# Kernel tuning notes

Measured on AMD Instinct MI355X. Metric: run time of the kernel, lower is better.

## Reference

```python
import jax, jax.numpy as jnp
import numpy as np

B, L, D = 2, 2048, 2560
H, KV, HD = 8, 4, 256
FF = 10240
WINDOW = 1024
ROPE_BASE = 10000.0
EPS = 1e-6


def rmsnorm(x, scale=None):
    x32 = x.astype(jnp.float32)
    var = jnp.mean(jnp.square(x32), axis=-1, keepdims=True)
    xn = x32 * jax.lax.rsqrt(var + EPS)
    return xn if scale is None else xn * scale.astype(jnp.float32)


def apply_rope(x, positions, base):
    # full RoPE (rope_fraction=1.0): rotate pairs (i, i+head_dim//2)
    hd = x.shape[-1]
    half = hd // 2
    timescale = base ** (2.0 * jnp.arange(half, dtype=jnp.float32) / hd)
    ang = positions[:, :, None].astype(jnp.float32) / timescale  # [B,L,half]
    sin = jnp.sin(ang)[:, :, None, :]  # [B,L,1,half]
    cos = jnp.cos(ang)[:, :, None, :]
    x1, x2 = x[..., :half], x[..., half:]
    return jnp.concatenate([x1 * cos - x2 * sin, x2 * cos + x1 * sin], axis=-1)


def setup_inputs() -> dict:
    key = jax.random.key(0)
    ks = jax.random.split(key, 16)
    s = lambda fan_in: 1.0 / np.sqrt(fan_in)
    return {
        "x": jax.random.normal(ks[0], (B, L, D), jnp.float32),
        "positions": jnp.broadcast_to(jnp.arange(L, dtype=jnp.int32), (B, L)),
        "wq": jax.random.normal(ks[1], (D, H * HD), jnp.float32) * s(D),
        "wk": jax.random.normal(ks[2], (D, KV * HD), jnp.float32) * s(D),
        "wv": jax.random.normal(ks[3], (D, KV * HD), jnp.float32) * s(D),
        "wo": jax.random.normal(ks[4], (H * HD, D), jnp.float32) * s(H * HD),
        "q_scale": jnp.ones((HD,), jnp.float32),
        "k_scale": jnp.ones((HD,), jnp.float32),
        "pre_attn_scale": jnp.ones((D,), jnp.float32),
        "post_attn_scale": jnp.ones((D,), jnp.float32),
        "pre_ffw_scale": jnp.ones((D,), jnp.float32),
        "post_ffw_scale": jnp.ones((D,), jnp.float32),
        "w_gate": jax.random.normal(ks[5], (D, FF), jnp.float32) * s(D),
        "w_up": jax.random.normal(ks[6], (D, FF), jnp.float32) * s(D),
        "w_down": jax.random.normal(ks[7], (FF, D), jnp.float32) * s(FF),
    }


def reference(x, positions, wq, wk, wv, wo, q_scale, k_scale,
              pre_attn_scale, post_attn_scale, pre_ffw_scale, post_ffw_scale,
              w_gate, w_up, w_down):
    # --- attention sub-block ---
    h = rmsnorm(x, pre_attn_scale)
    q = (h @ wq).reshape(B, L, H, HD)
    k = (h @ wk).reshape(B, L, KV, HD)
    v = (h @ wv).reshape(B, L, KV, HD)
    q = apply_rope(rmsnorm(q, q_scale), positions, ROPE_BASE)
    k = apply_rope(rmsnorm(k, k_scale), positions, ROPE_BASE)
    v = rmsnorm(v)  # RMSNormNoScale on V
    rep = H // KV
    k = jnp.repeat(k, rep, axis=2)  # [B,L,H,HD]
    v = jnp.repeat(v, rep, axis=2)
    scores = jnp.einsum("bqhd,bkhd->bhqk", q, k)  # NOTE: no 1/sqrt(d) scaling, faithful to source
    i = jnp.arange(L)[:, None]
    j = jnp.arange(L)[None, :]
    mask = (j <= i) & (j > i - WINDOW)  # causal & sliding window
    scores = jnp.where(mask[None, None, :, :], scores, -10000.0)
    probs = jax.nn.softmax(scores.astype(jnp.float32), axis=-1)
    attn = jnp.einsum("bhqk,bkhd->bqhd", probs, v).reshape(B, L, H * HD)
    attn = attn @ wo
    x = x + rmsnorm(attn, post_attn_scale)
    # --- feedforward sub-block (GeGLU) ---
    h = rmsnorm(x, pre_ffw_scale)
    hidden = jax.nn.gelu(h @ w_gate, approximate=False) * (h @ w_up)
    ffw = hidden @ w_down
    x = x + rmsnorm(ffw, post_ffw_scale)
    return x
```

## Files before the change

kernel.cpp:

```cpp
#include <hip/hip_runtime.h>
#include <math.h>

#define DEV __device__ __forceinline__

typedef _Float16 f16;
typedef _Float16 f16x8 __attribute__((ext_vector_type(8)));
typedef _Float16 f16x4 __attribute__((ext_vector_type(4)));
typedef float f32x4 __attribute__((ext_vector_type(4)));

DEV void gload_lds16(const void* g, void* l) {
  __builtin_amdgcn_global_load_lds(
      (const __attribute__((address_space(1))) void*)g,
      (__attribute__((address_space(3))) void*)l, 16, 0, 0);
}

__global__ void transpose_w(const float* __restrict__ src, f16* __restrict__ dst,
                            int R, int C) {
  __shared__ float tile[32][33];
  int c0 = blockIdx.x * 32, r0 = blockIdx.y * 32;
  int tx = threadIdx.x, ty = threadIdx.y;
#pragma unroll
  for (int j = 0; j < 32; j += 8)
    tile[ty + j][tx] = src[(size_t)(r0 + ty + j) * C + c0 + tx];
  __syncthreads();
#pragma unroll
  for (int j = 0; j < 32; j += 8)
    dst[(size_t)(c0 + ty + j) * R + r0 + tx] = (f16)tile[tx][ty + j];
}

__global__ void rope_table_k(float* __restrict__ tab) {
  int idx = blockIdx.x * 256 + threadIdx.x;
  int pos = idx >> 7, j = idx & 127;
  float ts = powf(10000.0f, (float)j * (1.0f / 128.0f));
  float ang = (float)pos / ts;
  tab[pos * 256 + j] = sinf(ang);
  tab[pos * 256 + 128 + j] = cosf(ang);
}

__global__ __launch_bounds__(256) void rmsnorm_f32_f16(
    const float* __restrict__ in, const float* __restrict__ scale,
    f16* __restrict__ out) {
  constexpr int D = 2560, N4 = D / 4;
  const int m = blockIdx.x, tid = threadIdx.x;
  const float* row = in + (size_t)m * D;
  float vals[12];
  float ss = 0.f;
#pragma unroll
  for (int it = 0; it < 3; ++it) {
    int c4 = tid + it * 256;
    if (c4 < N4) {
      float4 v = *(const float4*)(row + c4 * 4);
      vals[it * 4 + 0] = v.x; vals[it * 4 + 1] = v.y;
      vals[it * 4 + 2] = v.z; vals[it * 4 + 3] = v.w;
      ss += v.x * v.x + v.y * v.y + v.z * v.z + v.w * v.w;
    }
  }
#pragma unroll
  for (int off = 32; off; off >>= 1) ss += __shfl_xor(ss, off, 64);
  __shared__ float red[4];
  if ((tid & 63) == 0) red[tid >> 6] = ss;
  __syncthreads();
  float rs = rsqrtf((red[0] + red[1] + red[2] + red[3]) * (1.0f / D) + 1e-6f);
#pragma unroll
  for (int it = 0; it < 3; ++it) {
    int c4 = tid + it * 256;
    if (c4 < N4) {
      float4 sc = *(const float4*)(scale + c4 * 4);
      f16x4 o;
      o[0] = (f16)(vals[it * 4 + 0] * rs * sc.x);
      o[1] = (f16)(vals[it * 4 + 1] * rs * sc.y);
      o[2] = (f16)(vals[it * 4 + 2] * rs * sc.z);
      o[3] = (f16)(vals[it * 4 + 3] * rs * sc.w);
      *(f16x4*)(out + (size_t)m * D + c4 * 4) = o;
    }
  }
}

__global__ __launch_bounds__(256) void residual_rmsnorm(
    const float* x, const f16* __restrict__ y,
    const float* __restrict__ scale, float* out) {
  constexpr int D = 2560, N4 = D / 4;
  const int m = blockIdx.x, tid = threadIdx.x;
  const f16* yr = y + (size_t)m * D;
  float yv[12];
  float ss = 0.f;
#pragma unroll
  for (int it = 0; it < 3; ++it) {
    int c4 = tid + it * 256;
    if (c4 < N4) {
      f16x4 u = *(const f16x4*)(yr + c4 * 4);
      float a = (float)u[0], b = (float)u[1], c = (float)u[2], d = (float)u[3];
      yv[it * 4 + 0] = a; yv[it * 4 + 1] = b; yv[it * 4 + 2] = c; yv[it * 4 + 3] = d;
      ss += a * a + b * b + c * c + d * d;
    }
  }
#pragma unroll
  for (int off = 32; off; off >>= 1) ss += __shfl_xor(ss, off, 64);
  __shared__ float red[4];
  if ((tid & 63) == 0) red[tid >> 6] = ss;
  __syncthreads();
  float rs = rsqrtf((red[0] + red[1] + red[2] + red[3]) * (1.0f / D) + 1e-6f);
#pragma unroll
  for (int it = 0; it < 3; ++it) {
    int c4 = tid + it * 256;
    if (c4 < N4) {
      float4 xv = *(const float4*)(x + (size_t)m * D + c4 * 4);
      float4 sc = *(const float4*)(scale + c4 * 4);
      float4 o;
      o.x = xv.x + yv[it * 4 + 0] * rs * sc.x;
      o.y = xv.y + yv[it * 4 + 1] * rs * sc.y;
      o.z = xv.z + yv[it * 4 + 2] * rs * sc.z;
      o.w = xv.w + yv[it * 4 + 3] * rs * sc.w;
      *(float4*)(out + (size_t)m * D + c4 * 4) = o;
    }
  }
}

__global__ __launch_bounds__(256) void norm_rope_k(
    const f16* __restrict__ qkv, const int* __restrict__ positions,
    const float* __restrict__ q_scale, const float* __restrict__ k_scale,
    const float* __restrict__ tab,
    f16* __restrict__ q_g, f16* __restrict__ k_g, f16* __restrict__ v_n) {
  const int m = blockIdx.x;
  const int tid = threadIdx.x, w = tid >> 6, l = tid & 63;
  const int pos = positions[m];
  const float* srow = tab + (size_t)pos * 256;
  const int c0 = l * 4;
  for (int vi = w; vi < 16; vi += 4) {
    f16x4 u = *(const f16x4*)(qkv + (size_t)m * 4096 + vi * 256 + c0);
    float x0 = (float)u[0], x1 = (float)u[1], x2 = (float)u[2], x3 = (float)u[3];
    float ss = x0 * x0 + x1 * x1 + x2 * x2 + x3 * x3;
#pragma unroll
    for (int off = 32; off; off >>= 1) ss += __shfl_xor(ss, off, 64);
    float rs = rsqrtf(ss * (1.0f / 256.0f) + 1e-6f);
    if (vi < 12) {
      const float* sc = (vi < 8) ? q_scale : k_scale;
      float4 s4 = *(const float4*)(sc + c0);
      float n0 = x0 * rs * s4.x, n1 = x1 * rs * s4.y;
      float n2 = x2 * rs * s4.z, n3 = x3 * rs * s4.w;
      float p0 = __shfl_xor(n0, 32, 64), p1 = __shfl_xor(n1, 32, 64);
      float p2 = __shfl_xor(n2, 32, 64), p3 = __shfl_xor(n3, 32, 64);
      int j0 = c0 & 127;
      float4 sn = *(const float4*)(srow + j0);
      float4 cs = *(const float4*)(srow + 128 + j0);
      float sgn = (l < 32) ? -1.0f : 1.0f;
      f16x4 o;
      o[0] = (f16)(n0 * cs.x + sgn * p0 * sn.x);
      o[1] = (f16)(n1 * cs.y + sgn * p1 * sn.y);
      o[2] = (f16)(n2 * cs.z + sgn * p2 * sn.z);
      o[3] = (f16)(n3 * cs.w + sgn * p3 * sn.w);
      if (vi < 8) *(f16x4*)(q_g + (size_t)m * 2048 + vi * 256 + c0) = o;
      else        *(f16x4*)(k_g + (size_t)m * 1024 + (vi - 8) * 256 + c0) = o;
    } else {
      f16x4 o;
      o[0] = (f16)(x0 * rs); o[1] = (f16)(x1 * rs);
      o[2] = (f16)(x2 * rs); o[3] = (f16)(x3 * rs);
      *(f16x4*)(v_n + (size_t)m * 1024 + (vi - 12) * 256 + c0) = o;
    }
  }
}

__global__ void transpose_v_k(const f16* __restrict__ v_n, f16* __restrict__ vt) {
  __shared__ f16 tile[32][33];
  int bkv = blockIdx.z;
  int b = bkv >> 2, kv = bkv & 3;
  int t0 = blockIdx.x * 32, d0 = blockIdx.y * 32;
  int tx = threadIdx.x, ty = threadIdx.y;
#pragma unroll
  for (int j = 0; j < 32; j += 8)
    tile[ty + j][tx] =
        v_n[(size_t)(b * 2048 + t0 + ty + j) * 1024 + kv * 256 + d0 + tx];
  __syncthreads();
#pragma unroll
  for (int j = 0; j < 32; j += 8)
    vt[((size_t)bkv * 256 + d0 + ty + j) * 2048 + t0 + tx] = tile[tx][ty + j];
}

template <int EPI>
__global__ void gemm_bt(const f16* __restrict__ A, const f16* __restrict__ BT,
                        f16* C, const f16* aux, int M, int N, int K) {
  constexpr int BM = 128, BN = 128, BK = 64;
  __shared__ f16 As[BM * BK];
  __shared__ f16 Bs[BN * BK];
  const int tid = threadIdx.x;
  const int w = tid >> 6, l = tid & 63;
  const int l15 = l & 15, lk = l >> 4;
  const int bn = blockIdx.x, bm = blockIdx.y;
  const int wm = (w >> 1) * 64, wn = (w & 1) * 64;

  f32x4 acc[4][4] = {};

  const size_t abase = (size_t)(bm * BM) * K;
  const size_t bbase = (size_t)(bn * BN) * K;
  const int r = tid >> 3, cc = (tid & 7) * 8;

  for (int kt = 0; kt < K; kt += BK) {
#pragma unroll
    for (int it = 0; it < 4; ++it) {
      int rr = r + it * 32;
      gload_lds16(A + abase + (size_t)rr * K + kt + cc, &As[rr * BK + cc]);
      gload_lds16(BT + bbase + (size_t)rr * K + kt + cc, &Bs[rr * BK + cc]);
    }
    __syncthreads();
#pragma unroll
    for (int ks = 0; ks < 2; ++ks) {
      f16x8 af[4], bfr[4];
#pragma unroll
      for (int mi = 0; mi < 4; ++mi)
        af[mi] = *(const f16x8*)&As[(wm + mi * 16 + l15) * BK + ks * 32 + lk * 8];
#pragma unroll
      for (int ni = 0; ni < 4; ++ni)
        bfr[ni] = *(const f16x8*)&Bs[(wn + ni * 16 + l15) * BK + ks * 32 + lk * 8];
#pragma unroll
      for (int mi = 0; mi < 4; ++mi)
#pragma unroll
        for (int ni = 0; ni < 4; ++ni)
          acc[mi][ni] = __builtin_amdgcn_mfma_f32_16x16x32_f16(
              af[mi], bfr[ni], acc[mi][ni], 0, 0, 0);
    }
    __syncthreads();
  }
#pragma unroll
  for (int mi = 0; mi < 4; ++mi) {
#pragma unroll
    for (int ni = 0; ni < 4; ++ni) {
#pragma unroll
      for (int i = 0; i < 4; ++i) {
        int row = bm * BM + wm + mi * 16 + lk * 4 + i;
        int col = bn * BN + wn + ni * 16 + l15;
        size_t idx = (size_t)row * N + col;
        float v = acc[mi][ni][i];
        if constexpr (EPI == 1) {
          v = 0.5f * v * (1.0f + erff(v * 0.70710678118654752f));
        } else if constexpr (EPI == 2) {
          v *= (float)aux[idx];
        }
        C[idx] = (f16)v;
      }
    }
  }
}

__global__ __launch_bounds__(256) void flash_attn_k(
    const f16* __restrict__ q_g, const f16* __restrict__ k_g,
    const f16* __restrict__ vt, f16* __restrict__ ctx) {
  constexpr int KP = 264, VP = 40, PP = 40;
  __shared__ f16 Ks[32 * KP];
  __shared__ f16 Vs[256 * VP];
  __shared__ f16 Ps[4][16 * PP];
  const int qt = blockIdx.x, h = blockIdx.y, b = blockIdx.z;
  const int tid = threadIdx.x, w = tid >> 6, l = tid & 63;
  const int l15 = l & 15, lk = l >> 4;
  const int kv = h >> 1;

  f16x8 aq[8];
  const int qrow = qt * 64 + w * 16 + l15;
  const f16* qp = q_g + (size_t)(b * 2048 + qrow) * 2048 + h * 256 + lk * 8;
#pragma unroll
  for (int kc = 0; kc < 8; ++kc) aq[kc] = *(const f16x8*)(qp + kc * 32);

  f32x4 o[16] = {};
  float mrow[4] = {-1e30f, -1e30f, -1e30f, -1e30f};
  float lrow[4] = {0.f, 0.f, 0.f, 0.f};

  int kt_lo = 2 * qt - 32; if (kt_lo < 0) kt_lo = 0;
  const int kt_hi = 2 * qt + 1;
  const int iqb = qt * 64 + w * 16 + lk * 4;

  for (int kt = kt_lo; kt <= kt_hi; ++kt) {
    __syncthreads();
#pragma unroll
    for (int it = 0; it < 4; ++it) {
      int ch = tid + it * 256;
      int jl = ch >> 5, kcc = (ch & 31) * 8;
      *(f16x8*)&Ks[jl * KP + kcc] = *(const f16x8*)(
          k_g + (size_t)(b * 2048 + kt * 32 + jl) * 1024 + kv * 256 + kcc);
      int d = ch >> 2, tc = (ch & 3) * 8;
      *(f16x8*)&Vs[d * VP + tc] = *(const f16x8*)(
          vt + ((size_t)(b * 4 + kv) * 256 + d) * 2048 + kt * 32 + tc);
    }
    __syncthreads();
    f32x4 s[2] = {};
#pragma unroll
    for (int ct = 0; ct < 2; ++ct)
#pragma unroll
      for (int kc = 0; kc < 8; ++kc) {
        f16x8 bk = *(const f16x8*)&Ks[(ct * 16 + l15) * KP + kc * 32 + lk * 8];
        s[ct] = __builtin_amdgcn_mfma_f32_16x16x32_f16(aq[kc], bk, s[ct], 0, 0, 0);
      }
    float pm[4] = {-1e30f, -1e30f, -1e30f, -1e30f};
#pragma unroll
    for (int ct = 0; ct < 2; ++ct)
#pragma unroll
      for (int i = 0; i < 4; ++i) {
        int iq = iqb + i;
        int j = kt * 32 + ct * 16 + l15;
        bool valid = (j <= iq) && (j > iq - 1024);
        float sv = valid ? s[ct][i] : -1e30f;
        s[ct][i] = sv;
        pm[i] = fmaxf(pm[i], sv);
      }
#pragma unroll
    for (int i = 0; i < 4; ++i)
#pragma unroll
      for (int off = 1; off < 16; off <<= 1)
        pm[i] = fmaxf(pm[i], __shfl_xor(pm[i], off, 64));
    float corr[4], rsum[4];
#pragma unroll
    for (int i = 0; i < 4; ++i) {
      float mn = fmaxf(mrow[i], pm[i]);
      corr[i] = __expf(mrow[i] - mn);
      mrow[i] = mn;
      rsum[i] = 0.f;
    }
#pragma unroll
    for (int ct = 0; ct < 2; ++ct)
#pragma unroll
      for (int i = 0; i < 4; ++i) {
        float p = (s[ct][i] > -1e29f) ? __expf(s[ct][i] - mrow[i]) : 0.f;
        s[ct][i] = p;
        rsum[i] += p;
      }
#pragma unroll
    for (int i = 0; i < 4; ++i) {
#pragma unroll
      for (int off = 1; off < 16; off <<= 1) rsum[i] += __shfl_xor(rsum[i], off, 64);
      lrow[i] = lrow[i] * corr[i] + rsum[i];
    }
#pragma unroll
    for (int dt = 0; dt < 16; ++dt)
#pragma unroll
      for (int i = 0; i < 4; ++i) o[dt][i] *= corr[i];
#pragma unroll
    for (int ct = 0; ct < 2; ++ct)
#pragma unroll
      for (int i = 0; i < 4; ++i)
        Ps[w][(lk * 4 + i) * PP + ct * 16 + l15] = (f16)s[ct][i];
    __syncthreads();
    f16x8 pa = *(const f16x8*)&Ps[w][l15 * PP + lk * 8];
#pragma unroll
    for (int dt = 0; dt < 16; ++dt) {
      f16x8 bv = *(const f16x8*)&Vs[(dt * 16 + l15) * VP + lk * 8];
      o[dt] = __builtin_amdgcn_mfma_f32_16x16x32_f16(pa, bv, o[dt], 0, 0, 0);
    }
  }
  float inv[4];
#pragma unroll
  for (int i = 0; i < 4; ++i) inv[i] = 1.0f / lrow[i];
  f16* op = ctx + (size_t)(b * 2048 + qt * 64 + w * 16 + lk * 4) * 2048 + h * 256 + l15;
#pragma unroll
  for (int dt = 0; dt < 16; ++dt)
#pragma unroll
    for (int i = 0; i < 4; ++i)
      op[(size_t)i * 2048 + dt * 16] = (f16)(o[dt][i] * inv[i]);
}

extern "C" void kernel_launch(void* const* d_in, const int* in_sizes, int n_in,
                              void* d_out, int out_size, void* d_ws, size_t ws_size,
                              hipStream_t stream) {
  const float* x = (const float*)d_in[0];
  const int* positions = (const int*)d_in[1];
  const float* wq = (const float*)d_in[2];
  const float* wk = (const float*)d_in[3];
  const float* wv = (const float*)d_in[4];
  const float* wo = (const float*)d_in[5];
  const float* q_scale = (const float*)d_in[6];
  const float* k_scale = (const float*)d_in[7];
  const float* pre_attn = (const float*)d_in[8];
  const float* post_attn = (const float*)d_in[9];
  const float* pre_ffw = (const float*)d_in[10];
  const float* post_ffw = (const float*)d_in[11];
  const float* w_gate = (const float*)d_in[12];
  const float* w_up = (const float*)d_in[13];
  const float* w_down = (const float*)d_in[14];
  float* out = (float*)d_out;

  char* ws = (char*)d_ws;
  size_t off = 0;
  auto alloc = [&](size_t bytes) {
    char* p = ws + off;
    off += (bytes + 255) & ~(size_t)255;
    return p;
  };
  f16* wbuf = (f16*)alloc((size_t)10240 * 2560 * 2);
  float* tab = (float*)alloc((size_t)2048 * 256 * 4);
  f16* h     = (f16*)alloc((size_t)4096 * 2560 * 2);
  char* act  = alloc((size_t)92280832);
  f16* qkv    = (f16*)(act);
  f16* q_g    = (f16*)(act + (size_t)33554432);
  f16* k_g    = (f16*)(act + (size_t)33554432 + 16777216);
  f16* v_n    = (f16*)(act + (size_t)33554432 + 16777216 + 8388608);
  f16* vtb    = (f16*)(act + (size_t)33554432 + 16777216 + 2 * 8388608);
  f16* ctx    = (f16*)(act + (size_t)33554432 + 16777216 + 3 * 8388608);
  f16* attn_o = (f16*)(act);
  f16* gbuf = (f16*)(act);
  f16* ffw  = h;
  (void)in_sizes; (void)n_in; (void)out_size; (void)ws_size;

  dim3 tb(32, 8);
  rope_table_k<<<1024, 256, 0, stream>>>(tab);

  rmsnorm_f32_f16<<<4096, 256, 0, stream>>>(x, pre_attn, h);
  transpose_w<<<dim3(2048 / 32, 2560 / 32), tb, 0, stream>>>(wq, wbuf, 2560, 2048);
  transpose_w<<<dim3(1024 / 32, 2560 / 32), tb, 0, stream>>>(wk, wbuf + (size_t)2048 * 2560, 2560, 1024);
  transpose_w<<<dim3(1024 / 32, 2560 / 32), tb, 0, stream>>>(wv, wbuf + (size_t)3072 * 2560, 2560, 1024);
  gemm_bt<0><<<dim3(4096 / 128, 4096 / 128), 256, 0, stream>>>(h, wbuf, qkv, nullptr, 4096, 4096, 2560);
  norm_rope_k<<<4096, 256, 0, stream>>>(qkv, positions, q_scale, k_scale, tab, q_g, k_g, v_n);
  transpose_v_k<<<dim3(2048 / 32, 256 / 32, 8), tb, 0, stream>>>(v_n, vtb);
  flash_attn_k<<<dim3(32, 8, 2), 256, 0, stream>>>(q_g, k_g, vtb, ctx);
  transpose_w<<<dim3(2560 / 32, 2048 / 32), tb, 0, stream>>>(wo, wbuf, 2048, 2560);
  gemm_bt<0><<<dim3(2560 / 128, 4096 / 128), 256, 0, stream>>>(ctx, wbuf, attn_o, nullptr, 4096, 2560, 2048);
  residual_rmsnorm<<<4096, 256, 0, stream>>>(x, attn_o, post_attn, out);

  rmsnorm_f32_f16<<<4096, 256, 0, stream>>>(out, pre_ffw, h);
  transpose_w<<<dim3(10240 / 32, 2560 / 32), tb, 0, stream>>>(w_gate, wbuf, 2560, 10240);
  gemm_bt<1><<<dim3(10240 / 128, 4096 / 128), 256, 0, stream>>>(h, wbuf, gbuf, nullptr, 4096, 10240, 2560);
  transpose_w<<<dim3(10240 / 32, 2560 / 32), tb, 0, stream>>>(w_up, wbuf, 2560, 10240);
  gemm_bt<2><<<dim3(10240 / 128, 4096 / 128), 256, 0, stream>>>(h, wbuf, gbuf, gbuf, 4096, 10240, 2560);
  transpose_w<<<dim3(2560 / 32, 10240 / 32), tb, 0, stream>>>(w_down, wbuf, 10240, 2560);
  gemm_bt<0><<<dim3(2560 / 128, 4096 / 128), 256, 0, stream>>>(gbuf, wbuf, ffw, nullptr, 4096, 2560, 10240);
  residual_rmsnorm<<<4096, 256, 0, stream>>>(out, ffw, post_ffw, out);
}
```

Baseline: 1.291 ms.

## Replace 128x128 GEMM with pipelined 256x256 tile kernel using swizzled LDS

Replaces the simple 128x128 single-buffered GEMM with a 256x256-tile, 512-thread kernel. It uses 128KB of double-buffered dynamic LDS, an XOR-swizzled LDS layout, and staged async global-to-LDS loads interleaved with MFMA phases. It also adds a workgroup index swizzle for L2 locality and setprio around MFMA blocks. The goal is to hide global load latency, cut LDS bank conflicts and raise MFMA utilization across all projection and FFN GEMMs. The trade-off is fewer, larger workgroups (e.g. 160 blocks for N=2560) and heavy register and LDS pressure.

Measured after the change: 1.239 ms. -4.0%, faster.

```diff
diff --git a/kernel.cpp b/kernel.cpp
--- a/kernel.cpp
+++ b/kernel.cpp
@@ -177,57 +177,126 @@
 }
 
 template <int EPI>
-__global__ void gemm_bt(const f16* __restrict__ A, const f16* __restrict__ BT,
-                        f16* C, const f16* aux, int M, int N, int K) {
-  constexpr int BM = 128, BN = 128, BK = 64;
-  __shared__ f16 As[BM * BK];
-  __shared__ f16 Bs[BN * BK];
+__global__ __launch_bounds__(512, 2) void gemm256(
+    const f16* __restrict__ A, const f16* __restrict__ BT,
+    f16* __restrict__ C, const f16* __restrict__ aux, int M, int N, int K) {
+  extern __shared__ __align__(16) f16 lds[];
   const int tid = threadIdx.x;
   const int w = tid >> 6, l = tid & 63;
   const int l15 = l & 15, lk = l >> 4;
-  const int bn = blockIdx.x, bm = blockIdx.y;
-  const int wm = (w >> 1) * 64, wn = (w & 1) * 64;
-
-  f32x4 acc[4][4] = {};
-
-  const size_t abase = (size_t)(bm * BM) * K;
-  const size_t bbase = (size_t)(bn * BN) * K;
-  const int r = tid >> 3, cc = (tid & 7) * 8;
-
-  for (int kt = 0; kt < K; kt += BK) {
-#pragma unroll
-    for (int it = 0; it < 4; ++it) {
-      int rr = r + it * 32;
-      gload_lds16(A + abase + (size_t)rr * K + kt + cc, &As[rr * BK + cc]);
-      gload_lds16(BT + bbase + (size_t)rr * K + kt + cc, &Bs[rr * BK + cc]);
-    }
-    __syncthreads();
-#pragma unroll
-    for (int ks = 0; ks < 2; ++ks) {
-      f16x8 af[4], bfr[4];
-#pragma unroll
-      for (int mi = 0; mi < 4; ++mi)
-        af[mi] = *(const f16x8*)&As[(wm + mi * 16 + l15) * BK + ks * 32 + lk * 8];
+  const int wm = w >> 2, wn = w & 3;
+
+  const int gx = gridDim.x;
+  const int nwg = gx * gridDim.y;
+  const int orig = blockIdx.y * gx + blockIdx.x;
+  const int swz = (orig & 7) * (nwg >> 3) + (orig >> 3);
+  const int bn = swz % gx, bm = swz / gx;
+
+  const f16* Ab = A + (size_t)bm * 256 * K;
+  const f16* Bb = BT + (size_t)bn * 256 * K;
+  const int NT = K >> 6;
+
+  const int srow = tid >> 2;
+  const int sg = (tid & 3) ^ ((srow >> 1) & 3);
+
+  auto stage = [&](int op, int kh, int buf, int kt) {
+    const f16* src = (op ? Bb : Ab) + (size_t)srow * K + kt * 64 + kh * 32 + sg * 8;
+    f16* dst = lds + ((buf << 2) + (kh << 1) + op) * 8192 + tid * 8;
+    gload_lds16(src, dst);
+    gload_lds16(src + (size_t)128 * K, dst + 4096);
+  };
+
+  const int fcol = (lk ^ ((l15 >> 1) & 3)) << 3;
+  const int aoff = (wm * 128 + l15) * 32 + fcol;
+  const int boff = 8192 + (wn * 64 + l15) * 32 + fcol;
+
+  f32x4 acc[8][4] = {};
+
+  stage(0, 0, 0, 0);
+  stage(1, 0, 0, 0);
+  stage(0, 1, 0, 0);
+  stage(1, 1, 0, 0);
+  if (NT > 1) stage(0, 0, 1, 1);
+  asm volatile("s_waitcnt vmcnt(6)" ::: "memory");
+  __builtin_amdgcn_s_barrier();
+
+  for (int t = 0; t < NT; ++t) {
+    const int buf = t & 1, nbuf = buf ^ 1;
+    const f16* lb0 = lds + buf * 32768;
+    const f16* lb1 = lb0 + 16384;
+    f16x8 a[4], b[4];
+#pragma unroll
+    for (int i = 0; i < 4; ++i) a[i] = *(const f16x8*)(lb0 + aoff + i * 512);
+#pragma unroll
+    for (int i = 0; i < 4; ++i) b[i] = *(const f16x8*)(lb0 + boff + i * 512);
+    if (t + 1 < NT) stage(1, 0, nbuf, t + 1);
+    __builtin_amdgcn_s_barrier();
+    asm volatile("s_waitcnt lgkmcnt(0)" ::: "memory");
+    __builtin_amdgcn_sched_barrier(0);
+    __builtin_amdgcn_s_setprio(1);
+#pragma unroll
+    for (int mi = 0; mi < 4; ++mi)
 #pragma unroll
       for (int ni = 0; ni < 4; ++ni)
-        bfr[ni] = *(const f16x8*)&Bs[(wn + ni * 16 + l15) * BK + ks * 32 + lk * 8];
-#pragma unroll
-      for (int mi = 0; mi < 4; ++mi)
-#pragma unroll
-        for (int ni = 0; ni < 4; ++ni)
-          acc[mi][ni] = __builtin_amdgcn_mfma_f32_16x16x32_f16(
-              af[mi], bfr[ni], acc[mi][ni], 0, 0, 0);
-    }
-    __syncthreads();
-  }
-#pragma unroll
-  for (int mi = 0; mi < 4; ++mi) {
+        acc[mi][ni] = __builtin_amdgcn_mfma_f32_16x16x32_f16(a[mi], b[ni], acc[mi][ni], 0, 0, 0);
+    __builtin_amdgcn_s_setprio(0);
+    __builtin_amdgcn_s_barrier();
+#pragma unroll
+    for (int i = 0; i < 4; ++i) a[i] = *(const f16x8*)(lb0 + aoff + (4 + i) * 512);
+    if (t + 1 < NT) stage(0, 1, nbuf, t + 1);
+    __builtin_amdgcn_s_barrier();
+    asm volatile("s_waitcnt lgkmcnt(0)" ::: "memory");
+    __builtin_amdgcn_sched_barrier(0);
+    __builtin_amdgcn_s_setprio(1);
+#pragma unroll
+    for (int mi = 0; mi < 4; ++mi)
+#pragma unroll
+      for (int ni = 0; ni < 4; ++ni)
+        acc[4 + mi][ni] = __builtin_amdgcn_mfma_f32_16x16x32_f16(a[mi], b[ni], acc[4 + mi][ni], 0, 0, 0);
+    __builtin_amdgcn_s_setprio(0);
+    asm volatile("s_waitcnt vmcnt(6)" ::: "memory");
+    __builtin_amdgcn_s_barrier();
+#pragma unroll
+    for (int i = 0; i < 4; ++i) a[i] = *(const f16x8*)(lb1 + aoff + i * 512);
+#pragma unroll
+    for (int i = 0; i < 4; ++i) b[i] = *(const f16x8*)(lb1 + boff + i * 512);
+    if (t + 1 < NT) stage(1, 1, nbuf, t + 1);
+    __builtin_amdgcn_s_barrier();
+    asm volatile("s_waitcnt lgkmcnt(0)" ::: "memory");
+    __builtin_amdgcn_sched_barrier(0);
+    __builtin_amdgcn_s_setprio(1);
+#pragma unroll
+    for (int mi = 0; mi < 4; ++mi)
+#pragma unroll
+      for (int ni = 0; ni < 4; ++ni)
+        acc[mi][ni] = __builtin_amdgcn_mfma_f32_16x16x32_f16(a[mi], b[ni], acc[mi][ni], 0, 0, 0);
+    __builtin_amdgcn_s_setprio(0);
+    __builtin_amdgcn_s_barrier();
+#pragma unroll
+    for (int i = 0; i < 4; ++i) a[i] = *(const f16x8*)(lb1 + aoff + (4 + i) * 512);
+    if (t + 2 < NT) stage(0, 0, buf, t + 2);
+    __builtin_amdgcn_s_barrier();
+    asm volatile("s_waitcnt lgkmcnt(0)" ::: "memory");
+    __builtin_amdgcn_sched_barrier(0);
+    __builtin_amdgcn_s_setprio(1);
+#pragma unroll
+    for (int mi = 0; mi < 4; ++mi)
+#pragma unroll
+      for (int ni = 0; ni < 4; ++ni)
+        acc[4 + mi][ni] = __builtin_amdgcn_mfma_f32_16x16x32_f16(a[mi], b[ni], acc[4 + mi][ni], 0, 0, 0);
+    __builtin_amdgcn_s_setprio(0);
+    asm volatile("s_waitcnt vmcnt(6)" ::: "memory");
+    __builtin_amdgcn_s_barrier();
+  }
+
+#pragma unroll
+  for (int mi = 0; mi < 8; ++mi) {
 #pragma unroll
     for (int ni = 0; ni < 4; ++ni) {
 #pragma unroll
       for (int i = 0; i < 4; ++i) {
-        int row = bm * BM + wm + mi * 16 + lk * 4 + i;
-        int col = bn * BN + wn + ni * 16 + l15;
+        int row = bm * 256 + wm * 128 + mi * 16 + lk * 4 + i;
+        int col = bn * 256 + wn * 64 + ni * 16 + l15;
         size_t idx = (size_t)row * N + col;
         float v = acc[mi][ni][i];
         if constexpr (EPI == 1) {
@@ -374,6 +443,17 @@
   const float* w_up = (const float*)d_in[13];
   const float* w_down = (const float*)d_in[14];
   float* out = (float*)d_out;
+
+  static bool s_attr = []() {
+    hipFuncSetAttribute(reinterpret_cast<const void*>(&gemm256<0>),
+                        hipFuncAttributeMaxDynamicSharedMemorySize, 131072);
+    hipFuncSetAttribute(reinterpret_cast<const void*>(&gemm256<1>),
+                        hipFuncAttributeMaxDynamicSharedMemorySize, 131072);
+    hipFuncSetAttribute(reinterpret_cast<const void*>(&gemm256<2>),
+                        hipFuncAttributeMaxDynamicSharedMemorySize, 131072);
+    return true;
+  }();
+  (void)s_attr;
 
   char* ws = (char*)d_ws;
   size_t off = 0;
@@ -404,20 +484,20 @@
   transpose_w<<<dim3(2048 / 32, 2560 / 32), tb, 0, stream>>>(wq, wbuf, 2560, 2048);
   transpose_w<<<dim3(1024 / 32, 2560 / 32), tb, 0, stream>>>(wk, wbuf + (size_t)2048 * 2560, 2560, 1024);
   transpose_w<<<dim3(1024 / 32, 2560 / 32), tb, 0, stream>>>(wv, wbuf + (size_t)3072 * 2560, 2560, 1024);
-  gemm_bt<0><<<dim3(4096 / 128, 4096 / 128), 256, 0, stream>>>(h, wbuf, qkv, nullptr, 4096, 4096, 2560);
+  gemm256<0><<<dim3(4096 / 256, 4096 / 256), 512, 131072, stream>>>(h, wbuf, qkv, nullptr, 4096, 4096, 2560);
   norm_rope_k<<<4096, 256, 0, stream>>>(qkv, positions, q_scale, k_scale, tab, q_g, k_g, v_n);
   transpose_v_k<<<dim3(2048 / 32, 256 / 32, 8), tb, 0, stream>>>(v_n, vtb);
   flash_attn_k<<<dim3(32, 8, 2), 256, 0, stream>>>(q_g, k_g, vtb, ctx);
   transpose_w<<<dim3(2560 / 32, 2048 / 32), tb, 0, stream>>>(wo, wbuf, 2048, 2560);
-  gemm_bt<0><<<dim3(2560 / 128, 4096 / 128), 256, 0, stream>>>(ctx, wbuf, attn_o, nullptr, 4096, 2560, 2048);
+  gemm256<0><<<dim3(2560 / 256, 4096 / 256), 512, 131072, stream>>>(ctx, wbuf, attn_o, nullptr, 4096, 2560, 2048);
   residual_rmsnorm<<<4096, 256, 0, stream>>>(x, attn_o, post_attn, out);
 
   rmsnorm_f32_f16<<<4096, 256, 0, stream>>>(out, pre_ffw, h);
   transpose_w<<<dim3(10240 / 32, 2560 / 32), tb, 0, stream>>>(w_gate, wbuf, 2560, 10240);
-  gemm_bt<1><<<dim3(10240 / 128, 4096 / 128), 256, 0, stream>>>(h, wbuf, gbuf, nullptr, 4096, 10240, 2560);
+  gemm256<1><<<dim3(10240 / 256, 4096 / 256), 512, 131072, stream>>>(h, wbuf, gbuf, nullptr, 4096, 10240, 2560);
   transpose_w<<<dim3(10240 / 32, 2560 / 32), tb, 0, stream>>>(w_up, wbuf, 2560, 10240);
-  gemm_bt<2><<<dim3(10240 / 128, 4096 / 128), 256, 0, stream>>>(h, wbuf, gbuf, gbuf, 4096, 10240, 2560);
+  gemm256<2><<<dim3(10240 / 256, 4096 / 256), 512, 131072, stream>>>(h, wbuf, gbuf, gbuf, 4096, 10240, 2560);
   transpose_w<<<dim3(2560 / 32, 10240 / 32), tb, 0, stream>>>(w_down, wbuf, 10240, 2560);
-  gemm_bt<0><<<dim3(2560 / 128, 4096 / 128), 256, 0, stream>>>(gbuf, wbuf, ffw, nullptr, 4096, 2560, 10240);
+  gemm256<0><<<dim3(2560 / 256, 4096 / 256), 512, 131072, stream>>>(gbuf, wbuf, ffw, nullptr, 4096, 2560, 10240);
   residual_rmsnorm<<<4096, 256, 0, stream>>>(out, ffw, post_ffw, out);
 }
```
